# Kernel optimization log

Measured on AMD Instinct MI355X. Metric: run time of the kernel, lower is better.

## Reference

```python
import jax, jax.numpy as jnp
import numpy as np

EPS = 1e-8  # torch CosineSimilarity eps


def setup_inputs() -> dict:
    key = jax.random.key(0)
    ks = jax.random.split(key, 7)
    B, N, T, C, M, MEM, IN, E = 8, 512, 64, 128, 32, 20, 2, 4
    s = 0.05  # keep softmax logits in a sane range (xavier-like scale)
    return {
        "input": jax.random.normal(ks[0], (B, N, T, IN), jnp.float32),
        "hidden": jax.random.normal(ks[1], (E, B, N, T, C), jnp.float32),
        "memory": jax.random.normal(ks[2], (MEM, M), jnp.float32) * s,
        "input_query": jax.random.normal(ks[3], (IN, M), jnp.float32) * s,
        "Wq": jax.random.normal(ks[4], (E, C, M), jnp.float32) * s,
        "Wk": jax.random.normal(ks[5], (E, C, M), jnp.float32) * s,
        "Wv": jax.random.normal(ks[6], (E, C, M), jnp.float32) * s,
    }


def _cosine_sim(a, b):
    # torch.nn.CosineSimilarity(dim=-1): dot / (max(||a||,eps)*max(||b||,eps))
    num = jnp.sum(a * b, axis=-1)
    na = jnp.maximum(jnp.linalg.norm(a, axis=-1), EPS)
    nb = jnp.maximum(jnp.linalg.norm(b, axis=-1), EPS)
    return num / (na * nb)


def reference(input, hidden, memory, input_query, Wq, Wk, Wv):
    B, N, T, _ = input.shape
    out_dim = 1
    # query_mem: soft read from memory bank -> [B,N,T,mem_hid]
    q_in = jnp.einsum("bnti,im->bntm", input, input_query)
    mem_score = jax.nn.softmax(jnp.einsum("bntm,km->bntk", q_in, memory), axis=-1)
    memories = jnp.einsum("bntk,km->bntm", mem_score, memory)
    # per-expert self-attention over T (vectorized over the 4 experts)
    q = jnp.einsum("ebntc,ecm->ebntm", hidden, Wq)
    k = jnp.einsum("ebntc,ecm->ebntm", hidden, Wk)
    v = jnp.einsum("ebntc,ecm->ebntm", hidden, Wv)
    energy = jnp.einsum("ebntm,ebnsm->ebnts", q, k)  # [E,B,N,T,T]
    att = jnp.einsum("ebnts,ebnsm->ebntm", jax.nn.softmax(energy, axis=-1), v)
    # cosine similarity of memory read vs each expert's attended hidden
    scores = _cosine_sim(memories[None], att)  # [E,B,N,T]
    scores = jnp.moveaxis(scores, 0, -1)  # [B,N,T,E]
    out = jnp.broadcast_to(scores[..., None, :], (B, N, T, out_dim, scores.shape[-1]))
    return out
```

## Files before the change

kernel.cpp:

```cpp
#include <hip/hip_runtime.h>
#include <hip/hip_bf16.h>
#include <math.h>

#define Bc 8
#define Nc 512
#define Tc 64
#define Cc 128
#define Mc 32
#define MEMc 20
#define Ec 4

#define LDK  40
#define LDVT 72

#define UNITS 8

typedef short bf16x8 __attribute__((ext_vector_type(8)));
typedef float f32x4  __attribute__((ext_vector_type(4)));

__device__ __forceinline__ unsigned short f2bfu(float f) {
    return __builtin_bit_cast(unsigned short, __float2bfloat16(f));
}
__device__ __forceinline__ unsigned pk2bf(float x, float y) {
    return ((unsigned)f2bfu(y) << 16) | (unsigned)f2bfu(x);
}

__device__ __forceinline__ void gload_lds16(const void* g, void* l) {
    __builtin_amdgcn_global_load_lds(
        (const __attribute__((address_space(1))) unsigned int*)g,
        (__attribute__((address_space(3))) unsigned int*)l, 16, 0, 0);
}

__global__ void prep(const float* __restrict__ Wq, const float* __restrict__ Wk,
                     const float* __restrict__ Wv, const float* __restrict__ membank,
                     const float* __restrict__ iq,
                     short* __restrict__ wt_img, short* __restrict__ bankM,
                     float* __restrict__ G2) {
    const int t = threadIdx.x;
    if (blockIdx.x < 192) {
        int idx = blockIdx.x * 256 + t;
        int e   = idx / 12288;
        int r   = idx - e * 12288;
        int mat = r >> 12;
        int m   = (r >> 7) & 31;
        int c   = r & 127;
        const float* W = (mat == 0) ? Wq : (mat == 1) ? Wk : Wv;
        const int dst = e * 12288 + mat * 4096 + m * 128 + (c ^ ((m & 7) << 3));
        wt_img[dst] = (short)f2bfu(W[((size_t)e * Cc + c) * Mc + m]);
    } else {
        for (int idx = t; idx < Mc * 32; idx += 256) {
            int m = idx >> 5, k = idx & 31;
            bankM[idx] = (short)f2bfu((k < MEMc) ? membank[k * Mc + m] : 0.f);
        }
        if (t < MEMc) {
            float g0 = 0.f, g1 = 0.f;
            for (int m = 0; m < Mc; ++m) {
                float b = membank[t * Mc + m];
                g0 = fmaf(iq[m], b, g0);
                g1 = fmaf(iq[Mc + m], b, g1);
            }
            G2[2 * t]     = g0;
            G2[2 * t + 1] = g1;
        }
    }
}

__device__ __forceinline__ void load_hidden(const float* __restrict__ hrow, float4 h[8]) {
    #pragma unroll
    for (int kt = 0; kt < 4; ++kt) {
        h[2 * kt]     = *(const float4*)(hrow + kt * 32);
        h[2 * kt + 1] = *(const float4*)(hrow + kt * 32 + 4);
    }
}
__device__ __forceinline__ void conv_a(const float4 h[8], bf16x8 a[4]) {
    #pragma unroll
    for (int kt = 0; kt < 4; ++kt) {
        const float4 x = h[2 * kt], y = h[2 * kt + 1];
        a[kt] = __builtin_bit_cast(bf16x8, (uint4){pk2bf(x.x, x.y), pk2bf(x.z, x.w),
                                                   pk2bf(y.x, y.y), pk2bf(y.z, y.w)});
    }
}

__device__ __forceinline__ void proj_store(const short* __restrict__ sh_wt, const bf16x8 a[4],
                                           int lo, int hi, int w,
                                           short* __restrict__ sh_k, short* __restrict__ sh_vt,
                                           unsigned q_pk[4]) {
    f32x4 q_[2], k_[2], v_[2];
    #pragma unroll
    for (int nt = 0; nt < 2; ++nt)
        q_[nt] = k_[nt] = v_[nt] = (f32x4){0.f, 0.f, 0.f, 0.f};
    const int swz = (lo & 7) << 3;
    int col[4];
    #pragma unroll
    for (int kt = 0; kt < 4; ++kt) col[kt] = (kt * 32 + hi * 8) ^ swz;
    const short* wrow = sh_wt + lo * 128;
    #pragma unroll
    for (int nt = 0; nt < 2; ++nt) {
        const short* p0 = wrow + nt * 2048;
        #pragma unroll
        for (int kt = 0; kt < 4; ++kt) {
            const bf16x8 wq = *(const bf16x8*)(p0 + col[kt]);
            const bf16x8 wk = *(const bf16x8*)(p0 + 4096 + col[kt]);
            const bf16x8 wv = *(const bf16x8*)(p0 + 8192 + col[kt]);
            q_[nt] = __builtin_amdgcn_mfma_f32_16x16x32_bf16(wq, a[kt], q_[nt], 0, 0, 0);
            k_[nt] = __builtin_amdgcn_mfma_f32_16x16x32_bf16(wk, a[kt], k_[nt], 0, 0, 0);
            v_[nt] = __builtin_amdgcn_mfma_f32_16x16x32_bf16(wv, a[kt], v_[nt], 0, 0, 0);
        }
    }
    #pragma unroll
    for (int nt = 0; nt < 2; ++nt) {
        *(uint2*)&sh_k[(w * 16 + lo) * LDK + nt * 16 + hi * 4] =
            (uint2){pk2bf(k_[nt][0], k_[nt][1]), pk2bf(k_[nt][2], k_[nt][3])};
        #pragma unroll
        for (int j = 0; j < 4; ++j)
            sh_vt[(nt * 16 + hi * 4 + j) * LDVT + w * 16 + lo] = (short)f2bfu(v_[nt][j]);
        q_pk[nt * 2]     = pk2bf(q_[nt][0], q_[nt][1]);
        q_pk[nt * 2 + 1] = pk2bf(q_[nt][2], q_[nt][3]);
    }
}

__device__ __forceinline__ void gate_pd(const float* __restrict__ G2, float2 in2, unsigned pd[10]) {
    #pragma unroll
    for (int kp = 0; kp < 10; ++kp) {
        const float4 g = *(const float4*)(G2 + 4 * kp);
        pd[kp] = pk2bf(__expf(in2.x * g.x + in2.y * g.y),
                       __expf(in2.x * g.z + in2.y * g.w));
    }
}

__device__ __forceinline__ void mem_read(const short* __restrict__ bankM,
                                         const unsigned pd[10], int lo, int hi, int w,
                                         f32x4 am[2]) {
    am[0] = am[1] = (f32x4){0.f, 0.f, 0.f, 0.f};
    const int addrD = (w * 16 + lo) * 4;
    unsigned Wd[10];
    #pragma unroll
    for (int u = 0; u < 10; ++u)
        Wd[u] = __builtin_amdgcn_ds_bpermute(addrD, (int)pd[u]);
    unsigned b[4];
    #pragma unroll
    for (int u = 0; u < 4; ++u) {
        const unsigned l_ = (hi == 0) ? Wd[u] : Wd[4 + u];
        const unsigned h_ = (u < 2) ? ((hi == 2) ? Wd[8 + u] : 0u) : 0u;
        b[u] = (hi < 2) ? l_ : h_;
    }
    const bf16x8 bp2 = __builtin_bit_cast(bf16x8, (uint4){b[0], b[1], b[2], b[3]});
    #pragma unroll
    for (int nt = 0; nt < 2; ++nt) {
        const bf16x8 ab = *(const bf16x8*)(bankM + (nt * 16 + lo) * 32 + hi * 8);
        am[nt] = __builtin_amdgcn_mfma_f32_16x16x32_bf16(ab, bp2, am[nt], 0, 0, 0);
    }
}

__device__ __forceinline__ void attend_store(
    const short* __restrict__ shk, const short* __restrict__ shv,
    const unsigned q_pk[4], const f32x4 am[2],
    int lo, int hi, int w, int A01, int A23, int addrA, int addrB,
    int bn, int e, float* __restrict__ out) {
    unsigned pw[4][2];
    {
        unsigned l0 = __builtin_amdgcn_ds_bpermute(A01, (int)q_pk[0]);
        unsigned h0_ = __builtin_amdgcn_ds_bpermute(A01, (int)q_pk[2]);
        unsigned l1 = __builtin_amdgcn_ds_bpermute(A01, (int)q_pk[1]);
        unsigned h1_ = __builtin_amdgcn_ds_bpermute(A01, (int)q_pk[3]);
        unsigned l2 = __builtin_amdgcn_ds_bpermute(A23, (int)q_pk[0]);
        unsigned h2_ = __builtin_amdgcn_ds_bpermute(A23, (int)q_pk[2]);
        unsigned l3 = __builtin_amdgcn_ds_bpermute(A23, (int)q_pk[1]);
        unsigned h3_ = __builtin_amdgcn_ds_bpermute(A23, (int)q_pk[3]);
        const bf16x8 bq = __builtin_bit_cast(bf16x8, (uint4){
            (hi < 2) ? l0 : h0_, (hi < 2) ? l1 : h1_,
            (hi < 2) ? l2 : h2_, (hi < 2) ? l3 : h3_});
        #pragma unroll
        for (int st = 0; st < 4; ++st) {
            const bf16x8 akf = *(const bf16x8*)&shk[(st * 16 + lo) * LDK + hi * 8];
            const f32x4 en = __builtin_amdgcn_mfma_f32_16x16x32_bf16(
                akf, bq, (f32x4){0.f, 0.f, 0.f, 0.f}, 0, 0, 0);
            pw[st][0] = pk2bf(__expf(en[0]), __expf(en[1]));
            pw[st][1] = pk2bf(__expf(en[2]), __expf(en[3]));
        }
    }
    f32x4 av[2];
    av[0] = av[1] = (f32x4){0.f, 0.f, 0.f, 0.f};
    {
        bf16x8 bp[2];
        #pragma unroll
        for (int kt = 0; kt < 2; ++kt) {
            unsigned wrd[4];
            #pragma unroll
            for (int uu = 0; uu < 4; ++uu) {
                const int adr = (uu < 2) ? addrA : addrB;
                const unsigned ev = __builtin_amdgcn_ds_bpermute(adr, (int)pw[2 * kt][uu & 1]);
                const unsigned od = __builtin_amdgcn_ds_bpermute(adr, (int)pw[2 * kt + 1][uu & 1]);
                wrd[uu] = (hi < 2) ? ev : od;
            }
            bp[kt] = __builtin_bit_cast(bf16x8, (uint4){wrd[0], wrd[1], wrd[2], wrd[3]});
        }
        #pragma unroll
        for (int nt = 0; nt < 2; ++nt)
            #pragma unroll
            for (int kt = 0; kt < 2; ++kt) {
                const bf16x8 avt = *(const bf16x8*)&shv[(nt * 16 + lo) * LDVT + kt * 32 + hi * 8];
                av[nt] = __builtin_amdgcn_mfma_f32_16x16x32_bf16(avt, bp[kt], av[nt], 0, 0, 0);
            }
    }
    float d = 0.f, na = 0.f, nb = 0.f;
    #pragma unroll
    for (int nt = 0; nt < 2; ++nt)
        #pragma unroll
        for (int j = 0; j < 4; ++j) {
            const float av_ = av[nt][j], am_ = am[nt][j];
            d  = fmaf(av_, am_, d);
            na = fmaf(av_, av_, na);
            nb = fmaf(am_, am_, nb);
        }
    d  += __shfl_xor(d, 16);  d  += __shfl_xor(d, 32);
    na += __shfl_xor(na, 16); na += __shfl_xor(na, 32);
    nb += __shfl_xor(nb, 16); nb += __shfl_xor(nb, 32);
    if (hi == 0) {
        const float denom = fmaxf(sqrtf(na), 1e-8f) * fmaxf(sqrtf(nb), 1e-8f);
        out[((size_t)bn * Tc + w * 16 + lo) * Ec + e] = d / denom;
    }
}

__global__ __launch_bounds__(256, 4) void mg_mfma(
    const float* __restrict__ input,
    const float* __restrict__ hidden,
    const short* __restrict__ wt_img,
    const short* __restrict__ bankM,
    const float* __restrict__ G2,
    float* __restrict__ out)
{
    __shared__ __align__(16) short sh_wt[12288];
    __shared__ __align__(16) short sh_k [Tc * LDK];
    __shared__ __align__(16) short sh_vt[Mc * LDVT];

    const int t    = threadIdx.x;
    const int w    = t >> 6;
    const int lane = t & 63;
    const int lo   = lane & 15;
    const int hi   = lane >> 4;
    const int e    = blockIdx.x >> 9;
    const int bnb  = (blockIdx.x & 511) * UNITS;

    const int A01   = (((hi & 1) * 32) + lo) << 2;
    const int A23   = A01 + 64;
    const int addrA = (((hi & 1) * 2 + 0) * 16 + lo) * 4;
    const int addrB = (((hi & 1) * 2 + 1) * 16 + lo) * 4;

    {
        const short* gsrc = wt_img + (size_t)e * 12288 + w * 512 + lane * 8;
        short* ldst = sh_wt + w * 512;
        #pragma unroll
        for (int c = 0; c < 6; ++c)
            gload_lds16(gsrc + c * 2048, ldst + c * 2048);
    }

    float2 in2[UNITS];
    #pragma unroll
    for (int u = 0; u < UNITS; ++u)
        in2[u] = *(const float2*)(input + ((size_t)(bnb + u) * Tc + lane) * 2);

    const float* hbase = hidden + (((size_t)(e * 4096 + bnb)) * Tc + w * 16 + lo) * Cc + hi * 8;

    float4  h[8];
    bf16x8  a[4];
    unsigned q_pk[4];

    load_hidden(hbase, h);
    conv_a(h, a);
    __syncthreads();
    proj_store(sh_wt, a, lo, hi, w, sh_k, sh_vt, q_pk);
    __syncthreads();

#define PHASE(U, NOT_LAST) do {                                                   \
        if (NOT_LAST) load_hidden(hbase + (U + 1) * (Tc * Cc), h);                \
        unsigned pd[10];                                                          \
        gate_pd(G2, in2[U], pd);                                                  \
        f32x4 am[2];                                                              \
        mem_read(bankM, pd, lo, hi, w, am);                                       \
        attend_store(sh_k, sh_vt, q_pk, am, lo, hi, w, A01, A23, addrA, addrB,    \
                     bnb + U, e, out);                                            \
        if (NOT_LAST) {                                                           \
            conv_a(h, a);                                                         \
            __syncthreads();              \
            proj_store(sh_wt, a, lo, hi, w, sh_k, sh_vt, q_pk);                   \
            __syncthreads();                                  \
        }                                                                         \
    } while (0)

    PHASE(0, 1);
    PHASE(1, 1);
    PHASE(2, 1);
    PHASE(3, 1);
    PHASE(4, 1);
    PHASE(5, 1);
    PHASE(6, 1);
    PHASE(7, 0);
#undef PHASE
}

extern "C" void kernel_launch(void* const* d_in, const int* in_sizes, int n_in,
                              void* d_out, int out_size, void* d_ws, size_t ws_size,
                              hipStream_t stream) {
    const float* input   = (const float*)d_in[0];
    const float* hidden  = (const float*)d_in[1];
    const float* membank = (const float*)d_in[2];
    const float* iq      = (const float*)d_in[3];
    const float* Wq      = (const float*)d_in[4];
    const float* Wk      = (const float*)d_in[5];
    const float* Wv      = (const float*)d_in[6];
    float* out = (float*)d_out;

    short* wt_img = (short*)d_ws;
    short* bankM  = (short*)((char*)d_ws + 98304);
    float* G2     = (float*)((char*)d_ws + 100352);

    prep<<<193, 256, 0, stream>>>(Wq, Wk, Wv, membank, iq, wt_img, bankM, G2);
    mg_mfma<<<Ec * Bc * Nc / UNITS, 256, 0, stream>>>(input, hidden, wt_img, bankM, G2, out);
}
```

Measured before the change: 127.8 us.

## Give each wave its own (b,n) sequences to remove block-wide barriers

Each wave now handles two full (b,n) sequences on its own instead of all four waves splitting the 64 rows of one sequence. K and V^T go into a per-wave shared-memory slice, so the two __syncthreads per unit are removed and hidden loads are double-buffered across row tiles. This trades higher LDS use per block and more registers (launch bounds drop to 2 blocks per CU) for no inter-wave synchronization. The per-wave serial chain per sequence is longer, and occupancy may fall.

```diff
diff --git a/kernel.cpp b/kernel.cpp
--- a/kernel.cpp
+++ b/kernel.cpp
@@ -12,8 +12,7 @@
 
 #define LDK  40
 #define LDVT 72
-
-#define UNITS 8
+#define KVSZ (Tc * LDK + Mc * LDVT)
 
 typedef short bf16x8 __attribute__((ext_vector_type(8)));
 typedef float f32x4  __attribute__((ext_vector_type(4)));
@@ -65,11 +64,11 @@
     }
 }
 
-__device__ __forceinline__ void load_hidden(const float* __restrict__ hrow, float4 h[8]) {
+__device__ __forceinline__ void load8(const float* __restrict__ p, float4 h[8]) {
     #pragma unroll
     for (int kt = 0; kt < 4; ++kt) {
-        h[2 * kt]     = *(const float4*)(hrow + kt * 32);
-        h[2 * kt + 1] = *(const float4*)(hrow + kt * 32 + 4);
+        h[2 * kt]     = *(const float4*)(p + kt * 32);
+        h[2 * kt + 1] = *(const float4*)(p + kt * 32 + 4);
     }
 }
 __device__ __forceinline__ void conv_a(const float4 h[8], bf16x8 a[4]) {
@@ -81,10 +80,10 @@
     }
 }
 
-__device__ __forceinline__ void proj_store(const short* __restrict__ sh_wt, const bf16x8 a[4],
-                                           int lo, int hi, int w,
-                                           short* __restrict__ sh_k, short* __restrict__ sh_vt,
-                                           unsigned q_pk[4]) {
+__device__ __forceinline__ void proj_rt(const short* __restrict__ sh_wt, const bf16x8 a[4],
+                                        int lo, int hi, int rt,
+                                        short* __restrict__ myk, short* __restrict__ myv,
+                                        unsigned q_pk[4]) {
     f32x4 q_[2], k_[2], v_[2];
     #pragma unroll
     for (int nt = 0; nt < 2; ++nt)
@@ -109,11 +108,11 @@
     }
     #pragma unroll
     for (int nt = 0; nt < 2; ++nt) {
-        *(uint2*)&sh_k[(w * 16 + lo) * LDK + nt * 16 + hi * 4] =
+        *(uint2*)&myk[(rt * 16 + lo) * LDK + nt * 16 + hi * 4] =
             (uint2){pk2bf(k_[nt][0], k_[nt][1]), pk2bf(k_[nt][2], k_[nt][3])};
         #pragma unroll
         for (int j = 0; j < 4; ++j)
-            sh_vt[(nt * 16 + hi * 4 + j) * LDVT + w * 16 + lo] = (short)f2bfu(v_[nt][j]);
+            myv[(nt * 16 + hi * 4 + j) * LDVT + rt * 16 + lo] = (short)f2bfu(v_[nt][j]);
         q_pk[nt * 2]     = pk2bf(q_[nt][0], q_[nt][1]);
         q_pk[nt * 2 + 1] = pk2bf(q_[nt][2], q_[nt][3]);
     }
@@ -129,10 +128,10 @@
 }
 
 __device__ __forceinline__ void mem_read(const short* __restrict__ bankM,
-                                         const unsigned pd[10], int lo, int hi, int w,
+                                         const unsigned pd[10], int lo, int hi, int qt,
                                          f32x4 am[2]) {
     am[0] = am[1] = (f32x4){0.f, 0.f, 0.f, 0.f};
-    const int addrD = (w * 16 + lo) * 4;
+    const int addrD = (qt * 16 + lo) * 4;
     unsigned Wd[10];
     #pragma unroll
     for (int u = 0; u < 10; ++u)
@@ -153,9 +152,9 @@
 }
 
 __device__ __forceinline__ void attend_store(
-    const short* __restrict__ shk, const short* __restrict__ shv,
+    const short* __restrict__ myk, const short* __restrict__ myv,
     const unsigned q_pk[4], const f32x4 am[2],
-    int lo, int hi, int w, int A01, int A23, int addrA, int addrB,
+    int lo, int hi, int qt, int A01, int A23, int addrA, int addrB,
     int bn, int e, float* __restrict__ out) {
     unsigned pw[4][2];
     {
@@ -172,7 +171,7 @@
             (hi < 2) ? l2 : h2_, (hi < 2) ? l3 : h3_});
         #pragma unroll
         for (int st = 0; st < 4; ++st) {
-            const bf16x8 akf = *(const bf16x8*)&shk[(st * 16 + lo) * LDK + hi * 8];
+            const bf16x8 akf = *(const bf16x8*)&myk[(st * 16 + lo) * LDK + hi * 8];
             const f32x4 en = __builtin_amdgcn_mfma_f32_16x16x32_bf16(
                 akf, bq, (f32x4){0.f, 0.f, 0.f, 0.f}, 0, 0, 0);
             pw[st][0] = pk2bf(__expf(en[0]), __expf(en[1]));
@@ -199,7 +198,7 @@
         for (int nt = 0; nt < 2; ++nt)
             #pragma unroll
             for (int kt = 0; kt < 2; ++kt) {
-                const bf16x8 avt = *(const bf16x8*)&shv[(nt * 16 + lo) * LDVT + kt * 32 + hi * 8];
+                const bf16x8 avt = *(const bf16x8*)&myv[(nt * 16 + lo) * LDVT + kt * 32 + hi * 8];
                 av[nt] = __builtin_amdgcn_mfma_f32_16x16x32_bf16(avt, bp[kt], av[nt], 0, 0, 0);
             }
     }
@@ -218,11 +217,11 @@
     nb += __shfl_xor(nb, 16); nb += __shfl_xor(nb, 32);
     if (hi == 0) {
         const float denom = fmaxf(sqrtf(na), 1e-8f) * fmaxf(sqrtf(nb), 1e-8f);
-        out[((size_t)bn * Tc + w * 16 + lo) * Ec + e] = d / denom;
-    }
-}
-
-__global__ __launch_bounds__(256, 4) void mg_mfma(
+        out[((size_t)bn * Tc + qt * 16 + lo) * Ec + e] = d / denom;
+    }
+}
+
+__global__ __launch_bounds__(256, 2) void mg_mfma(
     const float* __restrict__ input,
     const float* __restrict__ hidden,
     const short* __restrict__ wt_img,
@@ -231,8 +230,7 @@
     float* __restrict__ out)
 {
     __shared__ __align__(16) short sh_wt[12288];
-    __shared__ __align__(16) short sh_k [Tc * LDK];
-    __shared__ __align__(16) short sh_vt[Mc * LDVT];
+    __shared__ __align__(16) short sh_kv[4][KVSZ];
 
     const int t    = threadIdx.x;
     const int w    = t >> 6;
@@ -240,7 +238,11 @@
     const int lo   = lane & 15;
     const int hi   = lane >> 4;
     const int e    = blockIdx.x >> 9;
-    const int bnb  = (blockIdx.x & 511) * UNITS;
+    const int bnA  = (blockIdx.x & 511) * 8 + w * 2;
+    const int bnB  = bnA + 1;
+
+    short* myk = sh_kv[w];
+    short* myv = sh_kv[w] + Tc * LDK;
 
     const int A01   = (((hi & 1) * 32) + lo) << 2;
     const int A23   = A01 + 64;
@@ -255,48 +257,55 @@
             gload_lds16(gsrc + c * 2048, ldst + c * 2048);
     }
 
-    float2 in2[UNITS];
-    #pragma unroll
-    for (int u = 0; u < UNITS; ++u)
-        in2[u] = *(const float2*)(input + ((size_t)(bnb + u) * Tc + lane) * 2);
-
-    const float* hbase = hidden + (((size_t)(e * 4096 + bnb)) * Tc + w * 16 + lo) * Cc + hi * 8;
-
-    float4  h[8];
-    bf16x8  a[4];
-    unsigned q_pk[4];
-
-    load_hidden(hbase, h);
-    conv_a(h, a);
+    const float* hbA = hidden + (((size_t)(e * 4096 + bnA)) * Tc + lo) * Cc + hi * 8;
+    const float* hbB = hbA + (size_t)Tc * Cc;
+
+    float4 hbuf0[8], hbuf1[8];
+    load8(hbA, hbuf0);
+    load8(hbA + 2048, hbuf1);
+    const float2 in2A = *(const float2*)(input + ((size_t)bnA * Tc + lane) * 2);
+    const float2 in2B = *(const float2*)(input + ((size_t)bnB * Tc + lane) * 2);
+
+    unsigned pd[10];
+    gate_pd(G2, in2A, pd);
+
     __syncthreads();
-    proj_store(sh_wt, a, lo, hi, w, sh_k, sh_vt, q_pk);
-    __syncthreads();
-
-#define PHASE(U, NOT_LAST) do {                                                   \
-        if (NOT_LAST) load_hidden(hbase + (U + 1) * (Tc * Cc), h);                \
-        unsigned pd[10];                                                          \
-        gate_pd(G2, in2[U], pd);                                                  \
-        f32x4 am[2];                                                              \
-        mem_read(bankM, pd, lo, hi, w, am);                                       \
-        attend_store(sh_k, sh_vt, q_pk, am, lo, hi, w, A01, A23, addrA, addrB,    \
-                     bnb + U, e, out);                                            \
-        if (NOT_LAST) {                                                           \
-            conv_a(h, a);                                                         \
-            __syncthreads();              \
-            proj_store(sh_wt, a, lo, hi, w, sh_k, sh_vt, q_pk);                   \
-            __syncthreads();                                  \
-        }                                                                         \
-    } while (0)
-
-    PHASE(0, 1);
-    PHASE(1, 1);
-    PHASE(2, 1);
-    PHASE(3, 1);
-    PHASE(4, 1);
-    PHASE(5, 1);
-    PHASE(6, 1);
-    PHASE(7, 0);
-#undef PHASE
+
+    unsigned q_pk[4][4];
+    bf16x8 a[4];
+
+    conv_a(hbuf0, a);  load8(hbA + 2 * 2048, hbuf0);
+    proj_rt(sh_wt, a, lo, hi, 0, myk, myv, q_pk[0]);
+    conv_a(hbuf1, a);  load8(hbA + 3 * 2048, hbuf1);
+    proj_rt(sh_wt, a, lo, hi, 1, myk, myv, q_pk[1]);
+    conv_a(hbuf0, a);  load8(hbB, hbuf0);
+    proj_rt(sh_wt, a, lo, hi, 2, myk, myv, q_pk[2]);
+    conv_a(hbuf1, a);  load8(hbB + 2048, hbuf1);
+    proj_rt(sh_wt, a, lo, hi, 3, myk, myv, q_pk[3]);
+
+    #pragma unroll
+    for (int qt = 0; qt < 4; ++qt) {
+        f32x4 am[2];
+        mem_read(bankM, pd, lo, hi, qt, am);
+        attend_store(myk, myv, q_pk[qt], am, lo, hi, qt, A01, A23, addrA, addrB, bnA, e, out);
+    }
+
+    gate_pd(G2, in2B, pd);
+    conv_a(hbuf0, a);  load8(hbB + 2 * 2048, hbuf0);
+    proj_rt(sh_wt, a, lo, hi, 0, myk, myv, q_pk[0]);
+    conv_a(hbuf1, a);  load8(hbB + 3 * 2048, hbuf1);
+    proj_rt(sh_wt, a, lo, hi, 1, myk, myv, q_pk[1]);
+    conv_a(hbuf0, a);
+    proj_rt(sh_wt, a, lo, hi, 2, myk, myv, q_pk[2]);
+    conv_a(hbuf1, a);
+    proj_rt(sh_wt, a, lo, hi, 3, myk, myv, q_pk[3]);
+
+    #pragma unroll
+    for (int qt = 0; qt < 4; ++qt) {
+        f32x4 am[2];
+        mem_read(bankM, pd, lo, hi, qt, am);
+        attend_store(myk, myv, q_pk[qt], am, lo, hi, qt, A01, A23, addrA, addrB, bnB, e, out);
+    }
 }
 
 extern "C" void kernel_launch(void* const* d_in, const int* in_sizes, int n_in,
@@ -316,5 +325,5 @@
     float* G2     = (float*)((char*)d_ws + 100352);
 
     prep<<<193, 256, 0, stream>>>(Wq, Wk, Wv, membank, iq, wt_img, bankM, G2);
-    mg_mfma<<<Ec * Bc * Nc / UNITS, 256, 0, stream>>>(input, hidden, wt_img, bankM, G2, out);
-}
+    mg_mfma<<<2048, 256, 0, stream>>>(input, hidden, wt_img, bankM, G2, out);
+}
```

New measurement: 144.3 us. 1.13x slower.

## Process two (b,n) units per 512-thread block instead of eight sequential units

Applied to the files above, without the earlier changes.

Replaces the persistent-style loop, where each 256-thread block processed eight (b,n) units in turn with software prefetch of the next hidden tile, with 512-thread blocks that each handle two units concurrently. Each unit gets its own K/V shared buffers. This removes the serial phase chain and its per-unit barriers and gives more blocks and waves. In exchange, each block loads the 24KB weight image for only two units instead of eight, which adds global-to-LDS traffic per unit, and the cross-unit prefetch overlap is lost.

```diff
diff --git a/kernel.cpp b/kernel.cpp
--- a/kernel.cpp
+++ b/kernel.cpp
@@ -12,8 +12,6 @@
 
 #define LDK  40
 #define LDVT 72
-
-#define UNITS 8
 
 typedef short bf16x8 __attribute__((ext_vector_type(8)));
 typedef float f32x4  __attribute__((ext_vector_type(4)));
@@ -65,27 +63,9 @@
     }
 }
 
-__device__ __forceinline__ void load_hidden(const float* __restrict__ hrow, float4 h[8]) {
-    #pragma unroll
-    for (int kt = 0; kt < 4; ++kt) {
-        h[2 * kt]     = *(const float4*)(hrow + kt * 32);
-        h[2 * kt + 1] = *(const float4*)(hrow + kt * 32 + 4);
-    }
-}
-__device__ __forceinline__ void conv_a(const float4 h[8], bf16x8 a[4]) {
-    #pragma unroll
-    for (int kt = 0; kt < 4; ++kt) {
-        const float4 x = h[2 * kt], y = h[2 * kt + 1];
-        a[kt] = __builtin_bit_cast(bf16x8, (uint4){pk2bf(x.x, x.y), pk2bf(x.z, x.w),
-                                                   pk2bf(y.x, y.y), pk2bf(y.z, y.w)});
-    }
-}
-
-__device__ __forceinline__ void proj_store(const short* __restrict__ sh_wt, const bf16x8 a[4],
-                                           int lo, int hi, int w,
-                                           short* __restrict__ sh_k, short* __restrict__ sh_vt,
-                                           unsigned q_pk[4]) {
-    f32x4 q_[2], k_[2], v_[2];
+__device__ __forceinline__ void proj(const short* __restrict__ sh_wt, const bf16x8* a,
+                                     int lo, int hi,
+                                     f32x4 q_[2], f32x4 k_[2], f32x4 v_[2]) {
     #pragma unroll
     for (int nt = 0; nt < 2; ++nt)
         q_[nt] = k_[nt] = v_[nt] = (f32x4){0.f, 0.f, 0.f, 0.f};
@@ -107,16 +87,6 @@
             v_[nt] = __builtin_amdgcn_mfma_f32_16x16x32_bf16(wv, a[kt], v_[nt], 0, 0, 0);
         }
     }
-    #pragma unroll
-    for (int nt = 0; nt < 2; ++nt) {
-        *(uint2*)&sh_k[(w * 16 + lo) * LDK + nt * 16 + hi * 4] =
-            (uint2){pk2bf(k_[nt][0], k_[nt][1]), pk2bf(k_[nt][2], k_[nt][3])};
-        #pragma unroll
-        for (int j = 0; j < 4; ++j)
-            sh_vt[(nt * 16 + hi * 4 + j) * LDVT + w * 16 + lo] = (short)f2bfu(v_[nt][j]);
-        q_pk[nt * 2]     = pk2bf(q_[nt][0], q_[nt][1]);
-        q_pk[nt * 2 + 1] = pk2bf(q_[nt][2], q_[nt][3]);
-    }
 }
 
 __device__ __forceinline__ void gate_pd(const float* __restrict__ G2, float2 in2, unsigned pd[10]) {
@@ -129,10 +99,10 @@
 }
 
 __device__ __forceinline__ void mem_read(const short* __restrict__ bankM,
-                                         const unsigned pd[10], int lo, int hi, int w,
+                                         const unsigned pd[10], int lo, int hi, int wu,
                                          f32x4 am[2]) {
     am[0] = am[1] = (f32x4){0.f, 0.f, 0.f, 0.f};
-    const int addrD = (w * 16 + lo) * 4;
+    const int addrD = (wu * 16 + lo) * 4;
     unsigned Wd[10];
     #pragma unroll
     for (int u = 0; u < 10; ++u)
@@ -155,7 +125,7 @@
 __device__ __forceinline__ void attend_store(
     const short* __restrict__ shk, const short* __restrict__ shv,
     const unsigned q_pk[4], const f32x4 am[2],
-    int lo, int hi, int w, int A01, int A23, int addrA, int addrB,
+    int lo, int hi, int wu, int A01, int A23, int addrA, int addrB,
     int bn, int e, float* __restrict__ out) {
     unsigned pw[4][2];
     {
@@ -218,11 +188,11 @@
     nb += __shfl_xor(nb, 16); nb += __shfl_xor(nb, 32);
     if (hi == 0) {
         const float denom = fmaxf(sqrtf(na), 1e-8f) * fmaxf(sqrtf(nb), 1e-8f);
-        out[((size_t)bn * Tc + w * 16 + lo) * Ec + e] = d / denom;
-    }
-}
-
-__global__ __launch_bounds__(256, 4) void mg_mfma(
+        out[((size_t)bn * Tc + wu * 16 + lo) * Ec + e] = d / denom;
+    }
+}
+
+__global__ __launch_bounds__(512, 6) void mg_mfma(
     const float* __restrict__ input,
     const float* __restrict__ hidden,
     const short* __restrict__ wt_img,
@@ -231,16 +201,18 @@
     float* __restrict__ out)
 {
     __shared__ __align__(16) short sh_wt[12288];
-    __shared__ __align__(16) short sh_k [Tc * LDK];
-    __shared__ __align__(16) short sh_vt[Mc * LDVT];
+    __shared__ __align__(16) short sh_k [2][Tc * LDK];
+    __shared__ __align__(16) short sh_vt[2][Mc * LDVT];
 
     const int t    = threadIdx.x;
     const int w    = t >> 6;
+    const int u    = w >> 2;
+    const int wu   = w & 3;
     const int lane = t & 63;
     const int lo   = lane & 15;
     const int hi   = lane >> 4;
-    const int e    = blockIdx.x >> 9;
-    const int bnb  = (blockIdx.x & 511) * UNITS;
+    const int e    = blockIdx.x >> 11;
+    const int bn   = (blockIdx.x & 2047) * 2 + u;
 
     const int A01   = (((hi & 1) * 32) + lo) << 2;
     const int A23   = A01 + 64;
@@ -251,52 +223,57 @@
         const short* gsrc = wt_img + (size_t)e * 12288 + w * 512 + lane * 8;
         short* ldst = sh_wt + w * 512;
         #pragma unroll
-        for (int c = 0; c < 6; ++c)
-            gload_lds16(gsrc + c * 2048, ldst + c * 2048);
-    }
-
-    float2 in2[UNITS];
-    #pragma unroll
-    for (int u = 0; u < UNITS; ++u)
-        in2[u] = *(const float2*)(input + ((size_t)(bnb + u) * Tc + lane) * 2);
-
-    const float* hbase = hidden + (((size_t)(e * 4096 + bnb)) * Tc + w * 16 + lo) * Cc + hi * 8;
-
-    float4  h[8];
-    bf16x8  a[4];
+        for (int c = 0; c < 3; ++c)
+            gload_lds16(gsrc + c * 4096, ldst + c * 4096);
+    }
+
+    const float2 in2 = *(const float2*)(input + ((size_t)bn * Tc + lane) * 2);
+    float4 h[8];
+    {
+        const float* hr = hidden + (((size_t)(e * 4096 + bn)) * Tc + wu * 16 + lo) * Cc + hi * 8;
+        #pragma unroll
+        for (int kt = 0; kt < 4; ++kt) {
+            h[2 * kt]     = *(const float4*)(hr + kt * 32);
+            h[2 * kt + 1] = *(const float4*)(hr + kt * 32 + 4);
+        }
+    }
+
+    f32x4 am[2];
+    {
+        unsigned pd[10];
+        gate_pd(G2, in2, pd);
+        mem_read(bankM, pd, lo, hi, wu, am);
+    }
+
+    bf16x8 a[4];
+    #pragma unroll
+    for (int kt = 0; kt < 4; ++kt) {
+        const float4 x = h[2 * kt], y = h[2 * kt + 1];
+        a[kt] = __builtin_bit_cast(bf16x8, (uint4){pk2bf(x.x, x.y), pk2bf(x.z, x.w),
+                                                   pk2bf(y.x, y.y), pk2bf(y.z, y.w)});
+    }
+
+    __syncthreads();
+
     unsigned q_pk[4];
-
-    load_hidden(hbase, h);
-    conv_a(h, a);
+    {
+        f32x4 q_[2], k_[2], v_[2];
+        proj(sh_wt, a, lo, hi, q_, k_, v_);
+        #pragma unroll
+        for (int nt = 0; nt < 2; ++nt) {
+            *(uint2*)&sh_k[u][(wu * 16 + lo) * LDK + nt * 16 + hi * 4] =
+                (uint2){pk2bf(k_[nt][0], k_[nt][1]), pk2bf(k_[nt][2], k_[nt][3])};
+            #pragma unroll
+            for (int j = 0; j < 4; ++j)
+                sh_vt[u][(nt * 16 + hi * 4 + j) * LDVT + wu * 16 + lo] = (short)f2bfu(v_[nt][j]);
+            q_pk[nt * 2]     = pk2bf(q_[nt][0], q_[nt][1]);
+            q_pk[nt * 2 + 1] = pk2bf(q_[nt][2], q_[nt][3]);
+        }
+    }
+
     __syncthreads();
-    proj_store(sh_wt, a, lo, hi, w, sh_k, sh_vt, q_pk);
-    __syncthreads();
-
-#define PHASE(U, NOT_LAST) do {                                                   \
-        if (NOT_LAST) load_hidden(hbase + (U + 1) * (Tc * Cc), h);                \
-        unsigned pd[10];                                                          \
-        gate_pd(G2, in2[U], pd);                                                  \
-        f32x4 am[2];                                                              \
-        mem_read(bankM, pd, lo, hi, w, am);                                       \
-        attend_store(sh_k, sh_vt, q_pk, am, lo, hi, w, A01, A23, addrA, addrB,    \
-                     bnb + U, e, out);                                            \
-        if (NOT_LAST) {                                                           \
-            conv_a(h, a);                                                         \
-            __syncthreads();              \
-            proj_store(sh_wt, a, lo, hi, w, sh_k, sh_vt, q_pk);                   \
-            __syncthreads();                                  \
-        }                                                                         \
-    } while (0)
-
-    PHASE(0, 1);
-    PHASE(1, 1);
-    PHASE(2, 1);
-    PHASE(3, 1);
-    PHASE(4, 1);
-    PHASE(5, 1);
-    PHASE(6, 1);
-    PHASE(7, 0);
-#undef PHASE
+
+    attend_store(sh_k[u], sh_vt[u], q_pk, am, lo, hi, wu, A01, A23, addrA, addrB, bn, e, out);
 }
 
 extern "C" void kernel_launch(void* const* d_in, const int* in_sizes, int n_in,
@@ -316,5 +293,5 @@
     float* G2     = (float*)((char*)d_ws + 100352);
 
     prep<<<193, 256, 0, stream>>>(Wq, Wk, Wv, membank, iq, wt_img, bankM, G2);
-    mg_mfma<<<Ec * Bc * Nc / UNITS, 256, 0, stream>>>(input, hidden, wt_img, bankM, G2, out);
-}
+    mg_mfma<<<Ec * Bc * Nc / 2, 512, 0, stream>>>(input, hidden, wt_img, bankM, G2, out);
+}
```

Result: faster. 119.4 us (-6.5%).
